# Performance work log

Measured on AMD Instinct MI355X. Metric: run time of the kernel, lower is better.

## Reference

```python
import jax, jax.numpy as jnp
import numpy as np

N = 100000      # nodes
E = 1600000     # edges (before self-loops)
T = 35          # temporal length
CT = 16         # temporal conv channels
H = 4           # heads
C = 32          # out channels per head
HC = H * C      # 128
B = 64          # graphs in batch
NEG = 0.2       # leaky relu slope (PyG default)


def _conv1d_relu(x, w, b, stride):
    # x: [N, Cin, L], w: [Cout, Cin, K]
    y = jax.lax.conv_general_dilated(x, w, (stride,), 'VALID',
                                     dimension_numbers=('NCH', 'OIH', 'NCH'))
    return jax.nn.relu(y + b[None, :, None])


def _gatv2(x, src, dst, ea, Wl, Wr, We, att, bias):
    # GATv2Conv (eval mode, add_self_loops=True, fill_value='mean')
    E0 = src.shape[0]
    deg = jax.ops.segment_sum(jnp.ones((E0,), x.dtype), dst, num_segments=N)
    loop_attr = jax.ops.segment_sum(ea, dst, num_segments=N) / jnp.maximum(deg, 1.0)[:, None]
    loops = jnp.arange(N)
    src2 = jnp.concatenate([src, loops])
    dst2 = jnp.concatenate([dst, loops])
    ea2 = jnp.concatenate([ea, loop_attr], axis=0)          # [E+N, 1]
    msg = (x @ Wl)[src2].reshape(-1, H, C)                   # x_j via lin_l
    tgt = (x @ Wr)[dst2].reshape(-1, H, C)                   # x_i via lin_r
    ef = (ea2 @ We).reshape(-1, H, C)                        # lin_edge
    s = jax.nn.leaky_relu(msg + tgt + ef, NEG)
    logits = jnp.einsum('ehc,hc->eh', s, att)                # [E+N, H]
    m = jax.ops.segment_max(logits, dst2, num_segments=N)    # every node has a self-loop
    p = jnp.exp(logits - m[dst2])
    denom = jax.ops.segment_sum(p, dst2, num_segments=N)
    alpha = p / denom[dst2]                                  # segment softmax
    out = jax.ops.segment_sum(msg * alpha[..., None], dst2, num_segments=N)
    return out.reshape(N, HC) + bias


def setup_inputs() -> dict:
    key = jax.random.key(0)
    ks = jax.random.split(key, 20)
    d = {}
    d['x'] = jax.random.normal(ks[0], (N, 1, T), dtype=jnp.float32)
    d['edge_index'] = jax.random.randint(ks[1], (2, E), 0, N)
    d['edge_attr'] = jax.random.normal(ks[2], (E, 1), dtype=jnp.float32)
    d['batch'] = jnp.sort(jax.random.randint(ks[3], (N,), 0, B))
    d['conv1_w'] = jax.random.normal(ks[4], (CT, 1, 3), dtype=jnp.float32) * 0.3
    d['conv1_b'] = jnp.zeros((CT,), jnp.float32)
    d['conv2_w'] = jax.random.normal(ks[5], (CT, CT, 3), dtype=jnp.float32) * 0.15
    d['conv2_b'] = jnp.zeros((CT,), jnp.float32)
    for i, pre in enumerate(['g1', 'g2']):
        kk = jax.random.split(ks[6 + i], 5)
        d[pre + '_Wl'] = jax.random.normal(kk[0], (HC, HC), dtype=jnp.float32) * (1.0 / np.sqrt(HC))
        d[pre + '_Wr'] = jax.random.normal(kk[1], (HC, HC), dtype=jnp.float32) * (1.0 / np.sqrt(HC))
        d[pre + '_We'] = jax.random.normal(kk[2], (1, HC), dtype=jnp.float32)
        d[pre + '_att'] = jax.random.normal(kk[3], (H, C), dtype=jnp.float32) * (1.0 / np.sqrt(C))
        d[pre + '_b'] = jnp.zeros((HC,), jnp.float32)
    d['fc_w'] = jax.random.normal(ks[8], (HC, 1), dtype=jnp.float32) * (1.0 / np.sqrt(HC))
    d['fc_b'] = jnp.zeros((1,), jnp.float32)
    return d


def reference(x, edge_index, edge_attr, batch,
              conv1_w, conv1_b, conv2_w, conv2_b,
              g1_Wl, g1_Wr, g1_We, g1_att, g1_b,
              g2_Wl, g2_Wr, g2_We, g2_att, g2_b,
              fc_w, fc_b):
    h = _conv1d_relu(x, conv1_w, conv1_b, 2)   # [N,16,17]
    h = _conv1d_relu(h, conv2_w, conv2_b, 2)   # [N,16,8]
    h = h.reshape(N, HC)
    src, dst = edge_index[0], edge_index[1]
    h = jax.nn.relu(_gatv2(h, src, dst, edge_attr, g1_Wl, g1_Wr, g1_We, g1_att, g1_b))
    h = jax.nn.relu(_gatv2(h, src, dst, edge_attr, g2_Wl, g2_Wr, g2_We, g2_att, g2_b))
    g = jax.ops.segment_sum(h, batch, num_segments=B)  # global_add_pool
    return (g @ fc_w + fc_b)[:, 0]
```

## Files before the change

### kernel.cpp

```cpp
#include <hip/hip_runtime.h>
#include <hip/hip_fp16.h>
#include <math.h>

#define NN 100000
#define EE 1600000
#define BB 64
#define CAP 48
#define EHALF 800000

#define CONV_B ((NN + 15) / 16)
#define SBH ((EHALF + 2047) / 2048)
#define CONVA_B (CONV_B + SBH)
#define GEMM_B ((NN + 63) / 64)
#define GEMMS_B (GEMM_B + SBH)
#define NODE_B ((NN + 255) / 256)

typedef _Float16 h2 __attribute__((ext_vector_type(2)));
typedef _Float16 f16x8 __attribute__((ext_vector_type(8)));
typedef float f32x4 __attribute__((ext_vector_type(4)));

__device__ __forceinline__ h2 h2bcast(float v) {
  _Float16 h = (_Float16)v; h2 r = { h, h }; return r;
}

__device__ __forceinline__ h2 lrelu_h2(h2 z) {
  const h2 c = { (_Float16)0.2f, (_Float16)0.2f };
  h2 zz = z * c;
#if __has_builtin(__builtin_elementwise_max)
  return __builtin_elementwise_max(z, zz);
#else
  h2 r; r.x = z.x > zz.x ? z.x : zz.x; r.y = z.y > zz.y ? z.y : zz.y; return r;
#endif
}

__device__ __forceinline__ void scatter8(int e0,
    const int* __restrict__ src, const int* __restrict__ dst,
    const float* __restrict__ ea, int* __restrict__ cursor,
    int2* __restrict__ pack)
{
  int4  d0 = *(const int4*)(dst + e0);
  int4  d1 = *(const int4*)(dst + e0 + 4);
  int4  s0 = *(const int4*)(src + e0);
  int4  s1 = *(const int4*)(src + e0 + 4);
  float4 a0 = *(const float4*)(ea + e0);
  float4 a1 = *(const float4*)(ea + e0 + 4);
  int p0 = atomicAdd(cursor + d0.x, 1);
  int p1 = atomicAdd(cursor + d0.y, 1);
  int p2 = atomicAdd(cursor + d0.z, 1);
  int p3 = atomicAdd(cursor + d0.w, 1);
  int p4 = atomicAdd(cursor + d1.x, 1);
  int p5 = atomicAdd(cursor + d1.y, 1);
  int p6 = atomicAdd(cursor + d1.z, 1);
  int p7 = atomicAdd(cursor + d1.w, 1);
  if (p0 < CAP) pack[(size_t)d0.x * CAP + p0] = make_int2(s0.x, __float_as_int(a0.x));
  if (p1 < CAP) pack[(size_t)d0.y * CAP + p1] = make_int2(s0.y, __float_as_int(a0.y));
  if (p2 < CAP) pack[(size_t)d0.z * CAP + p2] = make_int2(s0.z, __float_as_int(a0.z));
  if (p3 < CAP) pack[(size_t)d0.w * CAP + p3] = make_int2(s0.w, __float_as_int(a0.w));
  if (p4 < CAP) pack[(size_t)d1.x * CAP + p4] = make_int2(s1.x, __float_as_int(a1.x));
  if (p5 < CAP) pack[(size_t)d1.y * CAP + p5] = make_int2(s1.y, __float_as_int(a1.y));
  if (p6 < CAP) pack[(size_t)d1.z * CAP + p6] = make_int2(s1.z, __float_as_int(a1.z));
  if (p7 < CAP) pack[(size_t)d1.w * CAP + p7] = make_int2(s1.w, __float_as_int(a1.w));
}

__global__ __launch_bounds__(256) void wpack_kernel(
    const float* __restrict__ Wl0, const float* __restrict__ Wr0,
    const float* __restrict__ Wl1, const float* __restrict__ Wr1,
    unsigned int* __restrict__ Wp, int* __restrict__ cursor,
    int* __restrict__ gcnt)
{
  int t = blockIdx.x * 256 + threadIdx.x;
  if (t < NN) cursor[t] = 0;
  if (t < CAP + 1) gcnt[t] = 0;
  if (t < 32768) {
    int L = t >> 14;
    int rem = t & 16383;
    int ch = rem >> 6;
    int kk = rem & 63;
    const float* W = (L == 0) ? (ch < 128 ? Wl0 : Wr0) : (ch < 128 ? Wl1 : Wr1);
    int c = ch & 127;
    float v0 = W[(2 * kk) * 128 + c];
    float v1 = W[(2 * kk + 1) * 128 + c];
    h2 h = { (_Float16)v0, (_Float16)v1 };
    Wp[t] = __builtin_bit_cast(unsigned int, h);
  }
}

__global__ __launch_bounds__(256) void hist_kernel(
    const int* __restrict__ cursor, int* __restrict__ gcnt)
{
  __shared__ int hh[CAP + 1];
  int tid = threadIdx.x;
  if (tid <= CAP) hh[tid] = 0;
  __syncthreads();
  int n = blockIdx.x * 256 + tid;
  int c = -1;
  if (n < NN) {
    c = cursor[n]; if (c > CAP) c = CAP;
    atomicAdd(&hh[c], 1);
  }
  __syncthreads();
  if (tid <= CAP && hh[tid] > 0) atomicAdd(&gcnt[tid], hh[tid]);
}

__global__ __launch_bounds__(64) void prefix_kernel(
    const int* __restrict__ gcnt, int* __restrict__ gbase)
{
  if (threadIdx.x == 0) {
    int s = 0;
    for (int i = 0; i <= CAP; ++i) { gbase[i] = s; s += gcnt[i]; }
  }
}

__global__ __launch_bounds__(256) void place_kernel(
    const int* __restrict__ cursor, int* __restrict__ gbase,
    int* __restrict__ order)
{
  __shared__ int lh[CAP + 1];
  __shared__ int lb[CAP + 1];
  int tid = threadIdx.x;
  if (tid <= CAP) lh[tid] = 0;
  __syncthreads();
  int n = blockIdx.x * 256 + tid;
  int c = 0;
  if (n < NN) {
    c = cursor[n]; if (c > CAP) c = CAP;
    atomicAdd(&lh[c], 1);
  }
  __syncthreads();
  if (tid <= CAP) {
    int cnt = lh[tid];
    lb[tid] = cnt > 0 ? atomicAdd(&gbase[tid], cnt) : 0;
  }
  __syncthreads();
  if (tid <= CAP) lh[tid] = 0;
  __syncthreads();
  if (n < NN) {
    int s = atomicAdd(&lh[c], 1);
    order[lb[c] + s] = n;
  }
}

__global__ __launch_bounds__(256) void conv_scatter_kernel(
    const float* __restrict__ x,
    const float* __restrict__ w1, const float* __restrict__ b1,
    const float* __restrict__ w2, const float* __restrict__ b2,
    __half* __restrict__ h16,
    const int* __restrict__ src, const int* __restrict__ dst,
    const float* __restrict__ ea,
    int* __restrict__ cursor, int2* __restrict__ pack)
{
  int tid = threadIdx.x;
  int r17 = blockIdx.x % 17;
  if (r17 == 0) {
    int sid = blockIdx.x / 17;
    int e0 = sid * 2048 + tid * 8;
    if (e0 >= EHALF) return;
    scatter8(e0, src, dst, ea, cursor, pack);
    return;
  }
  int cid = (blockIdx.x / 17) * 16 + (r17 - 1);
  if (cid >= CONV_B) return;
  __shared__ float s_x[16 * 36];
  __shared__ float s_c1[16 * 272];
  int n0 = cid * 16;

  for (int i = tid; i < 16 * 35; i += 256)
    s_x[(i / 35) * 36 + (i % 35)] = x[(size_t)n0 * 35 + i];

  int node = tid >> 4;
  int lane = tid & 15;

  float w1a = w1[lane * 3], w1b = w1[lane * 3 + 1], w1c = w1[lane * 3 + 2];
  float bb1 = b1[lane];
  float bb2 = b2[lane];

  __syncthreads();

  const float* row = s_x + node * 36;
  float xr[36];
#pragma unroll
  for (int i = 0; i < 9; ++i)
    *(float4*)&xr[4 * i] = *(const float4*)&row[4 * i];

  float* c1n = s_c1 + node * 272;
#pragma unroll
  for (int p = 0; p < 17; ++p) {
    float a = fmaf(w1a, xr[2 * p], fmaf(w1b, xr[2 * p + 1], fmaf(w1c, xr[2 * p + 2], bb1)));
    c1n[p * 16 + lane] = fmaxf(a, 0.f);
  }

  float w2r[48];
#pragma unroll
  for (int i = 0; i < 12; ++i)
    *(float4*)&w2r[4 * i] = *(const float4*)&w2[lane * 48 + 4 * i];

  __syncthreads();

  float acc8[8];
#pragma unroll
  for (int t = 0; t < 8; ++t) {
    float acc = bb2;
#pragma unroll
    for (int k = 0; k < 3; ++k) {
      const float4* rp = (const float4*)(c1n + (2 * t + k) * 16);
      float4 r0 = rp[0], r1 = rp[1], r2 = rp[2], r3 = rp[3];
      acc = fmaf(w2r[0  + k], r0.x, acc);
      acc = fmaf(w2r[3  + k], r0.y, acc);
      acc = fmaf(w2r[6  + k], r0.z, acc);
      acc = fmaf(w2r[9  + k], r0.w, acc);
      acc = fmaf(w2r[12 + k], r1.x, acc);
      acc = fmaf(w2r[15 + k], r1.y, acc);
      acc = fmaf(w2r[18 + k], r1.z, acc);
      acc = fmaf(w2r[21 + k], r1.w, acc);
      acc = fmaf(w2r[24 + k], r2.x, acc);
      acc = fmaf(w2r[27 + k], r2.y, acc);
      acc = fmaf(w2r[30 + k], r2.z, acc);
      acc = fmaf(w2r[33 + k], r2.w, acc);
      acc = fmaf(w2r[36 + k], r3.x, acc);
      acc = fmaf(w2r[39 + k], r3.y, acc);
      acc = fmaf(w2r[42 + k], r3.z, acc);
      acc = fmaf(w2r[45 + k], r3.w, acc);
    }
    acc8[t] = fmaxf(acc, 0.f);
  }

  h2 q0 = { (_Float16)acc8[0], (_Float16)acc8[1] };
  h2 q1 = { (_Float16)acc8[2], (_Float16)acc8[3] };
  h2 q2 = { (_Float16)acc8[4], (_Float16)acc8[5] };
  h2 q3 = { (_Float16)acc8[6], (_Float16)acc8[7] };
  int4 pk;
  pk.x = __builtin_bit_cast(int, q0);
  pk.y = __builtin_bit_cast(int, q1);
  pk.z = __builtin_bit_cast(int, q2);
  pk.w = __builtin_bit_cast(int, q3);
  *(int4*)(h16 + (size_t)(n0 + node) * 128 + lane * 8) = pk;
}

__global__ __launch_bounds__(256) void gemm_dual(
    const __half* __restrict__ A16, const unsigned int* __restrict__ WpT,
    __half* __restrict__ Cl, __half* __restrict__ Cr,
    const int* __restrict__ src, const int* __restrict__ dst,
    const float* __restrict__ ea,
    int* __restrict__ cursor, int2* __restrict__ pack, int with_scatter)
{
  int tid = threadIdx.x;
  int gid = blockIdx.x;
  if (with_scatter) {
    int r5 = blockIdx.x % 5;
    if (r5 == 0) {
      int sid = blockIdx.x / 5;
      int e0 = EHALF + sid * 2048 + tid * 8;
      if (e0 >= EE) return;
      scatter8(e0, src, dst, ea, cursor, pack);
      return;
    }
    gid = (blockIdx.x / 5) * 4 + (r5 - 1);
    if (gid >= GEMM_B) return;
  }

  __shared__ uint4 sB[64 * 16];
  int row0 = gid * 64;
  for (int u = tid; u < 64 * 16; u += 256) {
    int node = u >> 4, cu = u & 15;
    uint4 v = { 0u, 0u, 0u, 0u };
    if (row0 + node < NN)
      v = *(const uint4*)(A16 + (size_t)(row0 + node) * 128 + cu * 8);
    sB[node * 16 + (cu ^ (node & 7))] = v;
  }
  __syncthreads();

  int wv = tid >> 6;
  int l  = tid & 63;
  int lr = l & 15;
  int lq = l >> 4;

  f32x4 acc[4][4];
#pragma unroll
  for (int ct = 0; ct < 4; ++ct)
#pragma unroll
    for (int nt = 0; nt < 4; ++nt)
      acc[ct][nt] = (f32x4){ 0.f, 0.f, 0.f, 0.f };

#pragma unroll
  for (int kc = 0; kc < 4; ++kc) {
    f16x8 afrag[4];
#pragma unroll
    for (int ct = 0; ct < 4; ++ct) {
      int ch = wv * 64 + ct * 16 + lr;
      int4 w = *(const int4*)(WpT + ch * 64 + kc * 16 + lq * 4);
      afrag[ct] = __builtin_bit_cast(f16x8, w);
    }
    f16x8 bfrag[4];
#pragma unroll
    for (int nt = 0; nt < 4; ++nt) {
      int node = nt * 16 + lr;
      int unit = kc * 4 + lq;
      uint4 v = sB[node * 16 + (unit ^ (node & 7))];
      bfrag[nt] = __builtin_bit_cast(f16x8, v);
    }
#pragma unroll
    for (int ct = 0; ct < 4; ++ct)
#pragma unroll
      for (int nt = 0; nt < 4; ++nt)
        acc[ct][nt] = __builtin_amdgcn_mfma_f32_16x16x32_f16(
            afrag[ct], bfrag[nt], acc[ct][nt], 0, 0, 0);
  }

  __half* Cb = (wv < 2) ? Cl : Cr;
#pragma unroll
  for (int ct = 0; ct < 4; ++ct) {
    int chm = ((wv & 1) * 64) + ct * 16 + lq * 4;
#pragma unroll
    for (int nt = 0; nt < 4; ++nt) {
      int node = row0 + nt * 16 + lr;
      if (node < NN) {
        h2 v0 = { (_Float16)acc[ct][nt][0], (_Float16)acc[ct][nt][1] };
        h2 v1 = { (_Float16)acc[ct][nt][2], (_Float16)acc[ct][nt][3] };
        uint2 u;
        u.x = __builtin_bit_cast(unsigned int, v0);
        u.y = __builtin_bit_cast(unsigned int, v1);
        *(uint2*)(Cb + (size_t)node * 128 + chm) = u;
      }
    }
  }
}

__device__ __forceinline__ float edge_logit16(const h2 m0, const h2 m1, const h2 m2, const h2 m3,
                                              h2 wh, const h2* hrd, const h2* we, const h2* at)
{
  h2 z0 = m0 + (hrd[0] + wh * we[0]);
  h2 z1 = m1 + (hrd[1] + wh * we[1]);
  h2 z2 = m2 + (hrd[2] + wh * we[2]);
  h2 z3 = m3 + (hrd[3] + wh * we[3]);
  h2 d = lrelu_h2(z0) * at[0];
  d = lrelu_h2(z1) * at[1] + d;
  d = lrelu_h2(z2) * at[2] + d;
  d = lrelu_h2(z3) * at[3] + d;
  float pf = (float)d.x + (float)d.y;
  pf += __shfl_xor(pf, 1, 4);
  pf += __shfl_xor(pf, 2, 4);
  return pf;
}

#define LOADM(dst, idx) { int4 raw_ = *(const int4*)(hl + (size_t)(idx) * 128 + j8); \
  dst##0 = __builtin_bit_cast(h2, raw_.x); dst##1 = __builtin_bit_cast(h2, raw_.y);  \
  dst##2 = __builtin_bit_cast(h2, raw_.z); dst##3 = __builtin_bit_cast(h2, raw_.w); }

__global__ __launch_bounds__(256) void gat_node_kernel(
    const int* __restrict__ order,
    const int* __restrict__ cnt_arr, const int2* __restrict__ pack,
    const __half* __restrict__ hl, const __half* __restrict__ hr,
    const float* __restrict__ We, const float* __restrict__ att,
    const float* __restrict__ bias, __half* __restrict__ out)
{
  int idx = blockIdx.x * 16 + (threadIdx.x >> 4);
  if (idx >= NN) return;
  int n = order[idx];
  int lq = threadIdx.x & 15;
  int j8 = lq * 8;

  const float RLN2 = 1.44269504088896340736f;
  int4 hraw = *(const int4*)(hr + (size_t)n * 128 + j8);
  h2 hrd[4] = { __builtin_bit_cast(h2, hraw.x), __builtin_bit_cast(h2, hraw.y),
                __builtin_bit_cast(h2, hraw.z), __builtin_bit_cast(h2, hraw.w) };
  float4 wf0 = *(const float4*)(We + j8);
  float4 wf1 = *(const float4*)(We + j8 + 4);
  h2 we[4] = { { (_Float16)wf0.x, (_Float16)wf0.y }, { (_Float16)wf0.z, (_Float16)wf0.w },
               { (_Float16)wf1.x, (_Float16)wf1.y }, { (_Float16)wf1.z, (_Float16)wf1.w } };
  float4 af0 = *(const float4*)(att + j8);
  float4 af1 = *(const float4*)(att + j8 + 4);
  h2 at[4] = { { (_Float16)(af0.x * RLN2), (_Float16)(af0.y * RLN2) },
               { (_Float16)(af0.z * RLN2), (_Float16)(af0.w * RLN2) },
               { (_Float16)(af1.x * RLN2), (_Float16)(af1.y * RLN2) },
               { (_Float16)(af1.z * RLN2), (_Float16)(af1.w * RLN2) } };

  int cnt = cnt_arr[n]; if (cnt > CAP) cnt = CAP;
  const int2* p = pack + (size_t)n * CAP;

  float m = -INFINITY, l = 0.f, wsum = 0.f;
  h2 zh = { (_Float16)0.f, (_Float16)0.f };
  h2 acc0 = zh, acc1 = zh, acc2 = zh, acc3 = zh;

  int nb = cnt >> 2;
  int4 ca = { 0, 0, 0, 0 }, cb = { 0, 0, 0, 0 };
  h2 nr10, nr11, nr12, nr13, nr20, nr21, nr22, nr23;
  h2 nr30, nr31, nr32, nr33, nr40, nr41, nr42, nr43;
  if (nb > 0) {
    const int4* p4 = (const int4*)p;
    ca = p4[0]; cb = p4[1];
    LOADM(nr1, ca.x); LOADM(nr2, ca.z); LOADM(nr3, cb.x); LOADM(nr4, cb.z);
  }
  for (int b = 0; b < nb; ++b) {
    int4 da = ca, db = cb;
    h2 m10 = nr10, m11 = nr11, m12 = nr12, m13 = nr13;
    h2 m20 = nr20, m21 = nr21, m22 = nr22, m23 = nr23;
    h2 m30 = nr30, m31 = nr31, m32 = nr32, m33 = nr33;
    h2 m40 = nr40, m41 = nr41, m42 = nr42, m43 = nr43;
    if (b + 1 < nb) {
      const int4* p4 = (const int4*)(p + (b + 1) * 4);
      ca = p4[0]; cb = p4[1];
      LOADM(nr1, ca.x); LOADM(nr2, ca.z); LOADM(nr3, cb.x); LOADM(nr4, cb.z);
    }
    float w1 = __int_as_float(da.y), w2 = __int_as_float(da.w);
    float w3 = __int_as_float(db.y), w4 = __int_as_float(db.w);
    wsum += (w1 + w2) + (w3 + w4);
    float p1 = edge_logit16(m10, m11, m12, m13, h2bcast(w1), hrd, we, at);
    float p2 = edge_logit16(m20, m21, m22, m23, h2bcast(w2), hrd, we, at);
    float p3 = edge_logit16(m30, m31, m32, m33, h2bcast(w3), hrd, we, at);
    float p4v = edge_logit16(m40, m41, m42, m43, h2bcast(w4), hrd, we, at);
    float mn = fmaxf(fmaxf(m, fmaxf(p1, p2)), fmaxf(p3, p4v));
    float sc = exp2f(m - mn);
    float t1 = exp2f(p1 - mn);
    float t2 = exp2f(p2 - mn);
    float t3 = exp2f(p3 - mn);
    float t4 = exp2f(p4v - mn);
    l = fmaf(l, sc, (t1 + t2) + (t3 + t4));
    h2 sch = h2bcast(sc);
    h2 t1h = h2bcast(t1), t2h = h2bcast(t2), t3h = h2bcast(t3), t4h = h2bcast(t4);
    acc0 = acc0 * sch + (t1h * m10 + (t2h * m20 + (t3h * m30 + t4h * m40)));
    acc1 = acc1 * sch + (t1h * m11 + (t2h * m21 + (t3h * m31 + t4h * m41)));
    acc2 = acc2 * sch + (t1h * m12 + (t2h * m22 + (t3h * m32 + t4h * m42)));
    acc3 = acc3 * sch + (t1h * m13 + (t2h * m23 + (t3h * m33 + t4h * m43)));
    m = mn;
  }
  for (int i = nb * 4; i < cnt; ++i) {
    int2 v1 = p[i];
    float w1 = __int_as_float(v1.y);
    h2 mm0, mm1, mm2, mm3;
    LOADM(mm, v1.x);
    wsum += w1;
    float p1 = edge_logit16(mm0, mm1, mm2, mm3, h2bcast(w1), hrd, we, at);
    float mn = fmaxf(m, p1);
    float sc = exp2f(m - mn);
    float t1 = exp2f(p1 - mn);
    l = fmaf(l, sc, t1);
    h2 sch = h2bcast(sc), t1h = h2bcast(t1);
    acc0 = acc0 * sch + t1h * mm0;
    acc1 = acc1 * sch + t1h * mm1;
    acc2 = acc2 * sch + t1h * mm2;
    acc3 = acc3 * sch + t1h * mm3;
    m = mn;
  }

  float la = wsum / fmaxf((float)cnt, 1.f);
  h2 sl0, sl1, sl2, sl3;
  LOADM(sl, n);
  float ps = edge_logit16(sl0, sl1, sl2, sl3, h2bcast(la), hrd, we, at);
  float mn = fmaxf(m, ps);
  float sc = exp2f(m - mn);
  float ts = exp2f(ps - mn);
  l = fmaf(l, sc, ts);
  h2 sch = h2bcast(sc), tsh = h2bcast(ts);
  acc0 = acc0 * sch + tsh * sl0;
  acc1 = acc1 * sch + tsh * sl1;
  acc2 = acc2 * sch + tsh * sl2;
  acc3 = acc3 * sch + tsh * sl3;

  float inv = 1.f / l;
  float4 b0 = *(const float4*)(bias + j8);
  float4 b1 = *(const float4*)(bias + j8 + 4);
  h2 o0 = { (_Float16)fmaxf(fmaf((float)acc0.x, inv, b0.x), 0.f),
            (_Float16)fmaxf(fmaf((float)acc0.y, inv, b0.y), 0.f) };
  h2 o1 = { (_Float16)fmaxf(fmaf((float)acc1.x, inv, b0.z), 0.f),
            (_Float16)fmaxf(fmaf((float)acc1.y, inv, b0.w), 0.f) };
  h2 o2 = { (_Float16)fmaxf(fmaf((float)acc2.x, inv, b1.x), 0.f),
            (_Float16)fmaxf(fmaf((float)acc2.y, inv, b1.y), 0.f) };
  h2 o3 = { (_Float16)fmaxf(fmaf((float)acc3.x, inv, b1.z), 0.f),
            (_Float16)fmaxf(fmaf((float)acc3.y, inv, b1.w), 0.f) };
  int4 pk;
  pk.x = __builtin_bit_cast(int, o0);
  pk.y = __builtin_bit_cast(int, o1);
  pk.z = __builtin_bit_cast(int, o2);
  pk.w = __builtin_bit_cast(int, o3);
  *(int4*)(out + (size_t)n * 128 + j8) = pk;
}

__global__ __launch_bounds__(128) void pool_kernel(
    const __half* __restrict__ h, const int* __restrict__ batch,
    float* __restrict__ pooled)
{
  int n0 = blockIdx.x * 64;
  if (n0 >= NN) return;
  int j = threadIdx.x;
  int nend = n0 + 64; if (nend > NN) nend = NN;
  float acc = 0.f;
  int curb = batch[n0];
  for (int n = n0; n < nend; ++n) {
    int b = batch[n];
    if (b != curb) {
      unsafeAtomicAdd(pooled + curb * 128 + j, acc);
      acc = 0.f; curb = b;
    }
    acc += __half2float(h[(size_t)n * 128 + j]);
  }
  unsafeAtomicAdd(pooled + curb * 128 + j, acc);
}

__global__ __launch_bounds__(128) void fc_kernel(
    const float* __restrict__ pooled, const float* __restrict__ fcw,
    const float* __restrict__ fcb, float* __restrict__ out)
{
  int b = blockIdx.x;
  int t = threadIdx.x;
  float v = pooled[b * 128 + t] * fcw[t];
#pragma unroll
  for (int off = 32; off >= 1; off >>= 1) v += __shfl_down(v, off, 64);
  __shared__ float sbuf[2];
  if ((t & 63) == 0) sbuf[t >> 6] = v;
  __syncthreads();
  if (t == 0) out[b] = sbuf[0] + sbuf[1] + fcb[0];
}

extern "C" void kernel_launch(void* const* d_in, const int* in_sizes, int n_in,
                              void* d_out, int out_size, void* d_ws, size_t ws_size,
                              hipStream_t stream)
{
  const float* x    = (const float*)d_in[0];
  const int*   ei   = (const int*)d_in[1];
  const float* ea   = (const float*)d_in[2];
  const int*   batch= (const int*)d_in[3];
  const float* c1w  = (const float*)d_in[4];
  const float* c1b  = (const float*)d_in[5];
  const float* c2w  = (const float*)d_in[6];
  const float* c2b  = (const float*)d_in[7];
  const float* gWl[2] = { (const float*)d_in[8],  (const float*)d_in[13] };
  const float* gWr[2] = { (const float*)d_in[9],  (const float*)d_in[14] };
  const float* gWe[2] = { (const float*)d_in[10], (const float*)d_in[15] };
  const float* gAt[2] = { (const float*)d_in[11], (const float*)d_in[16] };
  const float* gB [2] = { (const float*)d_in[12], (const float*)d_in[17] };
  const float* fcw  = (const float*)d_in[18];
  const float* fcb  = (const float*)d_in[19];
  float* out = (float*)d_out;

  const int* src = ei;
  const int* dst = ei + EE;

  __half* h16    = (__half*)d_ws;
  __half* hl     = h16 + (size_t)NN * 128;
  __half* hr     = hl + (size_t)NN * 128;
  int2*  pack    = (int2*)(hr + (size_t)NN * 128);
  int*   cursor  = (int*)(pack + (size_t)NN * CAP);
  float* pooled  = (float*)(cursor + NN);
  unsigned int* Wp = (unsigned int*)(pooled + BB * 128);
  int*   order   = (int*)(Wp + 32768);
  int*   gcnt    = order + NN;
  int*   gbase   = gcnt + (CAP + 1);

  hipMemsetAsync(pooled, 0, BB * 128 * sizeof(float), stream);

  wpack_kernel<<<NODE_B, 256, 0, stream>>>(gWl[0], gWr[0], gWl[1], gWr[1],
                                           Wp, cursor, gcnt);

  conv_scatter_kernel<<<CONVA_B, 256, 0, stream>>>(
      x, c1w, c1b, c2w, c2b, h16, src, dst, ea, cursor, pack);

  gemm_dual<<<GEMMS_B, 256, 0, stream>>>(
      h16, Wp, hl, hr, src, dst, ea, cursor, pack, 1);

  hist_kernel<<<NODE_B, 256, 0, stream>>>(cursor, gcnt);
  prefix_kernel<<<1, 64, 0, stream>>>(gcnt, gbase);
  place_kernel<<<NODE_B, 256, 0, stream>>>(cursor, gbase, order);

  gat_node_kernel<<<(NN + 15) / 16, 256, 0, stream>>>(order, cursor, pack, hl, hr,
                                                      gWe[0], gAt[0], gB[0], h16);

  gemm_dual<<<GEMM_B, 256, 0, stream>>>(
      h16, Wp + 16384, hl, hr, src, dst, ea, cursor, pack, 0);
  gat_node_kernel<<<(NN + 15) / 16, 256, 0, stream>>>(order, cursor, pack, hl, hr,
                                                      gWe[1], gAt[1], gB[1], h16);

  pool_kernel<<<(NN + 63) / 64, 128, 0, stream>>>(h16, batch, pooled);
  fc_kernel<<<BB, 128, 0, stream>>>(pooled, fcw, fcb, out);
}
```

Before: 422.8 us.

## Process eight edges per step with double-buffered prefetch, rebalance scatter split

New measurement: 440.4 us. 1.04x slower.

```diff
diff --git a/kernel.cpp b/kernel.cpp
--- a/kernel.cpp
+++ b/kernel.cpp
@@ -6,13 +6,14 @@
 #define EE 1600000
 #define BB 64
 #define CAP 48
-#define EHALF 800000
+#define ESPLIT 1048576
 
 #define CONV_B ((NN + 15) / 16)
-#define SBH ((EHALF + 2047) / 2048)
-#define CONVA_B (CONV_B + SBH)
+#define SA_B (ESPLIT / 2048)
+#define CONVA_B (13 * ((CONV_B + 11) / 12))
 #define GEMM_B ((NN + 63) / 64)
-#define GEMMS_B (GEMM_B + SBH)
+#define SB_B (((EE - ESPLIT) + 2047) / 2048)
+#define GEMMS_B (7 * SB_B)
 #define NODE_B ((NN + 255) / 256)
 
 typedef _Float16 h2 __attribute__((ext_vector_type(2)));
@@ -66,11 +67,12 @@
     const float* __restrict__ Wl0, const float* __restrict__ Wr0,
     const float* __restrict__ Wl1, const float* __restrict__ Wr1,
     unsigned int* __restrict__ Wp, int* __restrict__ cursor,
-    int* __restrict__ gcnt)
+    int* __restrict__ gcnt, float* __restrict__ pooled)
 {
   int t = blockIdx.x * 256 + threadIdx.x;
   if (t < NN) cursor[t] = 0;
   if (t < CAP + 1) gcnt[t] = 0;
+  if (t < BB * 128) pooled[t] = 0.f;
   if (t < 32768) {
     int L = t >> 14;
     int rem = t & 16383;
@@ -93,9 +95,8 @@
   if (tid <= CAP) hh[tid] = 0;
   __syncthreads();
   int n = blockIdx.x * 256 + tid;
-  int c = -1;
   if (n < NN) {
-    c = cursor[n]; if (c > CAP) c = CAP;
+    int c = cursor[n]; if (c > CAP) c = CAP;
     atomicAdd(&hh[c], 1);
   }
   __syncthreads();
@@ -150,15 +151,15 @@
     int* __restrict__ cursor, int2* __restrict__ pack)
 {
   int tid = threadIdx.x;
-  int r17 = blockIdx.x % 17;
-  if (r17 == 0) {
-    int sid = blockIdx.x / 17;
+  int r13 = blockIdx.x % 13;
+  if (r13 == 0) {
+    int sid = blockIdx.x / 13;
     int e0 = sid * 2048 + tid * 8;
-    if (e0 >= EHALF) return;
+    if (e0 >= ESPLIT) return;
     scatter8(e0, src, dst, ea, cursor, pack);
     return;
   }
-  int cid = (blockIdx.x / 17) * 16 + (r17 - 1);
+  int cid = (blockIdx.x / 13) * 12 + (r13 - 1);
   if (cid >= CONV_B) return;
   __shared__ float s_x[16 * 36];
   __shared__ float s_c1[16 * 272];
@@ -246,15 +247,15 @@
   int tid = threadIdx.x;
   int gid = blockIdx.x;
   if (with_scatter) {
-    int r5 = blockIdx.x % 5;
-    if (r5 == 0) {
-      int sid = blockIdx.x / 5;
-      int e0 = EHALF + sid * 2048 + tid * 8;
+    int r7 = blockIdx.x % 7;
+    if (r7 == 0) {
+      int sid = blockIdx.x / 7;
+      int e0 = ESPLIT + sid * 2048 + tid * 8;
       if (e0 >= EE) return;
       scatter8(e0, src, dst, ea, cursor, pack);
       return;
     }
-    gid = (blockIdx.x / 5) * 4 + (r5 - 1);
+    gid = (blockIdx.x / 7) * 6 + (r7 - 1);
     if (gid >= GEMM_B) return;
   }
 
@@ -345,6 +346,40 @@
 #define LOADM(dst, idx) { int4 raw_ = *(const int4*)(hl + (size_t)(idx) * 128 + j8); \
   dst##0 = __builtin_bit_cast(h2, raw_.x); dst##1 = __builtin_bit_cast(h2, raw_.y);  \
   dst##2 = __builtin_bit_cast(h2, raw_.z); dst##3 = __builtin_bit_cast(h2, raw_.w); }
+
+#define EL(Mp, w) edge_logit16(Mp##0, Mp##1, Mp##2, Mp##3, h2bcast(w), hrd, we, at)
+
+#define LOAD8(P, base) { const int4* p4_ = (const int4*)(p + (base)); \
+  P##c0 = p4_[0]; P##c1 = p4_[1]; P##c2 = p4_[2]; P##c3 = p4_[3]; \
+  LOADM(P##m0, P##c0.x); LOADM(P##m1, P##c0.z); LOADM(P##m2, P##c1.x); LOADM(P##m3, P##c1.z); \
+  LOADM(P##m4, P##c2.x); LOADM(P##m5, P##c2.z); LOADM(P##m6, P##c3.x); LOADM(P##m7, P##c3.z); }
+
+#define PROC8(P) { \
+  float w1 = __int_as_float(P##c0.y), w2 = __int_as_float(P##c0.w); \
+  float w3 = __int_as_float(P##c1.y), w4 = __int_as_float(P##c1.w); \
+  float w5 = __int_as_float(P##c2.y), w6 = __int_as_float(P##c2.w); \
+  float w7 = __int_as_float(P##c3.y), w8 = __int_as_float(P##c3.w); \
+  wsum += ((w1 + w2) + (w3 + w4)) + ((w5 + w6) + (w7 + w8)); \
+  float q1 = EL(P##m0, w1), q2 = EL(P##m1, w2), q3 = EL(P##m2, w3), q4 = EL(P##m3, w4); \
+  float q5 = EL(P##m4, w5), q6 = EL(P##m5, w6), q7 = EL(P##m6, w7), q8 = EL(P##m7, w8); \
+  float mx = fmaxf(fmaxf(fmaxf(q1, q2), fmaxf(q3, q4)), fmaxf(fmaxf(q5, q6), fmaxf(q7, q8))); \
+  float mn = fmaxf(m, mx); \
+  float sc = exp2f(m - mn); \
+  float t1 = exp2f(q1 - mn), t2 = exp2f(q2 - mn), t3 = exp2f(q3 - mn), t4 = exp2f(q4 - mn); \
+  float t5 = exp2f(q5 - mn), t6 = exp2f(q6 - mn), t7 = exp2f(q7 - mn), t8 = exp2f(q8 - mn); \
+  l = fmaf(l, sc, ((t1 + t2) + (t3 + t4)) + ((t5 + t6) + (t7 + t8))); \
+  h2 sch = h2bcast(sc); \
+  h2 T1 = h2bcast(t1), T2 = h2bcast(t2), T3 = h2bcast(t3), T4 = h2bcast(t4); \
+  h2 T5 = h2bcast(t5), T6 = h2bcast(t6), T7 = h2bcast(t7), T8 = h2bcast(t8); \
+  acc0 = acc0 * sch + (((T1 * P##m00 + T2 * P##m10) + (T3 * P##m20 + T4 * P##m30)) + \
+                       ((T5 * P##m40 + T6 * P##m50) + (T7 * P##m60 + T8 * P##m70))); \
+  acc1 = acc1 * sch + (((T1 * P##m01 + T2 * P##m11) + (T3 * P##m21 + T4 * P##m31)) + \
+                       ((T5 * P##m41 + T6 * P##m51) + (T7 * P##m61 + T8 * P##m71))); \
+  acc2 = acc2 * sch + (((T1 * P##m02 + T2 * P##m12) + (T3 * P##m22 + T4 * P##m32)) + \
+                       ((T5 * P##m42 + T6 * P##m52) + (T7 * P##m62 + T8 * P##m72))); \
+  acc3 = acc3 * sch + (((T1 * P##m03 + T2 * P##m13) + (T3 * P##m23 + T4 * P##m33)) + \
+                       ((T5 * P##m43 + T6 * P##m53) + (T7 * P##m63 + T8 * P##m73))); \
+  m = mn; }
 
 __global__ __launch_bounds__(256) void gat_node_kernel(
     const int* __restrict__ order,
@@ -381,55 +416,36 @@
   h2 zh = { (_Float16)0.f, (_Float16)0.f };
   h2 acc0 = zh, acc1 = zh, acc2 = zh, acc3 = zh;
 
-  int nb = cnt >> 2;
-  int4 ca = { 0, 0, 0, 0 }, cb = { 0, 0, 0, 0 };
-  h2 nr10, nr11, nr12, nr13, nr20, nr21, nr22, nr23;
-  h2 nr30, nr31, nr32, nr33, nr40, nr41, nr42, nr43;
-  if (nb > 0) {
-    const int4* p4 = (const int4*)p;
-    ca = p4[0]; cb = p4[1];
-    LOADM(nr1, ca.x); LOADM(nr2, ca.z); LOADM(nr3, cb.x); LOADM(nr4, cb.z);
-  }
-  for (int b = 0; b < nb; ++b) {
-    int4 da = ca, db = cb;
-    h2 m10 = nr10, m11 = nr11, m12 = nr12, m13 = nr13;
-    h2 m20 = nr20, m21 = nr21, m22 = nr22, m23 = nr23;
-    h2 m30 = nr30, m31 = nr31, m32 = nr32, m33 = nr33;
-    h2 m40 = nr40, m41 = nr41, m42 = nr42, m43 = nr43;
-    if (b + 1 < nb) {
-      const int4* p4 = (const int4*)(p + (b + 1) * 4);
-      ca = p4[0]; cb = p4[1];
-      LOADM(nr1, ca.x); LOADM(nr2, ca.z); LOADM(nr3, cb.x); LOADM(nr4, cb.z);
-    }
-    float w1 = __int_as_float(da.y), w2 = __int_as_float(da.w);
-    float w3 = __int_as_float(db.y), w4 = __int_as_float(db.w);
-    wsum += (w1 + w2) + (w3 + w4);
-    float p1 = edge_logit16(m10, m11, m12, m13, h2bcast(w1), hrd, we, at);
-    float p2 = edge_logit16(m20, m21, m22, m23, h2bcast(w2), hrd, we, at);
-    float p3 = edge_logit16(m30, m31, m32, m33, h2bcast(w3), hrd, we, at);
-    float p4v = edge_logit16(m40, m41, m42, m43, h2bcast(w4), hrd, we, at);
-    float mn = fmaxf(fmaxf(m, fmaxf(p1, p2)), fmaxf(p3, p4v));
-    float sc = exp2f(m - mn);
-    float t1 = exp2f(p1 - mn);
-    float t2 = exp2f(p2 - mn);
-    float t3 = exp2f(p3 - mn);
-    float t4 = exp2f(p4v - mn);
-    l = fmaf(l, sc, (t1 + t2) + (t3 + t4));
-    h2 sch = h2bcast(sc);
-    h2 t1h = h2bcast(t1), t2h = h2bcast(t2), t3h = h2bcast(t3), t4h = h2bcast(t4);
-    acc0 = acc0 * sch + (t1h * m10 + (t2h * m20 + (t3h * m30 + t4h * m40)));
-    acc1 = acc1 * sch + (t1h * m11 + (t2h * m21 + (t3h * m31 + t4h * m41)));
-    acc2 = acc2 * sch + (t1h * m12 + (t2h * m22 + (t3h * m32 + t4h * m42)));
-    acc3 = acc3 * sch + (t1h * m13 + (t2h * m23 + (t3h * m33 + t4h * m43)));
-    m = mn;
-  }
-  for (int i = nb * 4; i < cnt; ++i) {
+  int4 Ac0, Ac1, Ac2, Ac3, Bc0, Bc1, Bc2, Bc3;
+  h2 Am00, Am01, Am02, Am03, Am10, Am11, Am12, Am13;
+  h2 Am20, Am21, Am22, Am23, Am30, Am31, Am32, Am33;
+  h2 Am40, Am41, Am42, Am43, Am50, Am51, Am52, Am53;
+  h2 Am60, Am61, Am62, Am63, Am70, Am71, Am72, Am73;
+  h2 Bm00, Bm01, Bm02, Bm03, Bm10, Bm11, Bm12, Bm13;
+  h2 Bm20, Bm21, Bm22, Bm23, Bm30, Bm31, Bm32, Bm33;
+  h2 Bm40, Bm41, Bm42, Bm43, Bm50, Bm51, Bm52, Bm53;
+  h2 Bm60, Bm61, Bm62, Bm63, Bm70, Bm71, Bm72, Bm73;
+
+  int nb8 = cnt >> 3;
+  if (nb8 > 0) {
+    LOAD8(A, 0);
+    int b = 0;
+    for (;;) {
+      if (b + 1 < nb8) { LOAD8(B, (b + 1) * 8); }
+      PROC8(A);
+      ++b; if (b >= nb8) break;
+      if (b + 1 < nb8) { LOAD8(A, (b + 1) * 8); }
+      PROC8(B);
+      ++b; if (b >= nb8) break;
+    }
+  }
+  for (int i = nb8 * 8; i < cnt; ++i) {
     int2 v1 = p[i];
     float w1 = __int_as_float(v1.y);
     h2 mm0, mm1, mm2, mm3;
     LOADM(mm, v1.x);
     wsum += w1;
-    float p1 = edge_logit16(mm0, mm1, mm2, mm3, h2bcast(w1), hrd, we, at);
+    float p1 = EL(mm, w1);
     float mn = fmaxf(m, p1);
     float sc = exp2f(m - mn);
     float t1 = exp2f(p1 - mn);
@@ -445,7 +461,7 @@
   float la = wsum / fmaxf((float)cnt, 1.f);
   h2 sl0, sl1, sl2, sl3;
   LOADM(sl, n);
-  float ps = edge_logit16(sl0, sl1, sl2, sl3, h2bcast(la), hrd, we, at);
+  float ps = EL(sl, la);
   float mn = fmaxf(m, ps);
   float sc = exp2f(m - mn);
   float ts = exp2f(ps - mn);
@@ -546,10 +562,8 @@
   int*   gcnt    = order + NN;
   int*   gbase   = gcnt + (CAP + 1);
 
-  hipMemsetAsync(pooled, 0, BB * 128 * sizeof(float), stream);
-
   wpack_kernel<<<NODE_B, 256, 0, stream>>>(gWl[0], gWr[0], gWl[1], gWr[1],
-                                           Wp, cursor, gcnt);
+                                           Wp, cursor, gcnt, pooled);
 
   conv_scatter_kernel<<<CONVA_B, 256, 0, stream>>>(
       x, c1w, c1b, c2w, c2b, h16, src, dst, ea, cursor, pack);
```
